# Performance work log

Hardware: AMD Instinct MI355X
Metric: run time of the kernel (lower is better)

## Reference

```python
import jax, jax.numpy as jnp
import numpy as np

BITS = 50

def _xor(a, b):
    # binary XOR on {0,1} floats: a + b - 2ab
    return a + b - 2.0 * a * b

def _maj(a, b, c):
    # majority (carry-out of a full adder) on {0,1} floats
    return a * b + a * c + b * c - 2.0 * a * b * c

def setup_inputs() -> dict:
    key = jax.random.key(0)
    kA, kB = jax.random.split(key)
    N = 1_000_000
    A = jax.random.randint(kA, (N, BITS), 0, 2).astype(jnp.float32)
    B = jax.random.randint(kB, (N, BITS), 0, 2).astype(jnp.float32)
    return {"A": A, "B": B}

def reference(A, B):
    """A - B via two's complement ripple-carry: A + NOT(B) + 1, LSB first.
    Returns (result [..., 50], borrow [..., 1])."""
    not_b = 1.0 - B                      # VecNOT
    # scan over the 50 bits (sequential carry dependency)
    a_bits = jnp.moveaxis(A, -1, 0)      # [50, N]
    b_bits = jnp.moveaxis(not_b, -1, 0)  # [50, N]
    c0 = jnp.ones(A.shape[:-1], dtype=A.dtype)  # initial carry = 1

    def step(c, ab):
        a, b = ab
        s = _xor(_xor(a, b), c)          # FullAdder sum
        c_next = _maj(a, b, c)           # FullAdder carry
        return c_next, s

    c_final, sums = jax.lax.scan(step, c0, (a_bits, b_bits))
    result = jnp.moveaxis(sums, 0, -1)   # [N, 50]
    borrow = (1.0 - c_final)[..., None]  # borrow_not(carry), [N, 1]
    return result, borrow
```

## Files before the change

kernel.cpp:

```cpp
#include <hip/hip_runtime.h>


constexpr int BITS = 50;
constexpr unsigned long long MASK50 = (1ULL << BITS) - 1ULL;

__device__ __forceinline__ void gl_lds16(const float* g, float* l) {
    __builtin_amdgcn_global_load_lds(
        (const __attribute__((address_space(1))) void*)g,
        (__attribute__((address_space(3))) void*)l, 16, 0, 0);
}
__device__ __forceinline__ void gl_lds4(const float* g, float* l) {
    __builtin_amdgcn_global_load_lds(
        (const __attribute__((address_space(1))) void*)g,
        (__attribute__((address_space(3))) void*)l, 4, 0, 0);
}

__global__ __launch_bounds__(64) void Subtractor50Bit_kernel(
    const float* __restrict__ A, const float* __restrict__ B,
    float* __restrict__ out, int N)
{
    __shared__ float sA[3200];
    __shared__ float sB[3200];

    const int lane = threadIdx.x;
    const long long rowBase = (long long)blockIdx.x * 64;
    if (rowBase >= N) return;

    if (rowBase + 64 <= N) {
        const long long eBase = rowBase * BITS;
        const float* ga = A + eBase;
        const float* gb = B + eBase;

        #pragma unroll
        for (int j = 0; j < 12; ++j) gl_lds16(ga + 256 * j + 4 * lane, &sA[256 * j]);
        gl_lds4(ga + 3072 + lane, &sA[3072]);
        gl_lds4(ga + 3136 + lane, &sA[3136]);
        #pragma unroll
        for (int j = 0; j < 12; ++j) gl_lds16(gb + 256 * j + 4 * lane, &sB[256 * j]);
        gl_lds4(gb + 3072 + lane, &sB[3072]);
        gl_lds4(gb + 3136 + lane, &sB[3136]);

        asm volatile("s_waitcnt vmcnt(0)" ::: "memory");
        __builtin_amdgcn_sched_barrier(0);

        const float2* rA = (const float2*)sA + 25 * lane;
        const float2* rB = (const float2*)sB + 25 * lane;
        unsigned alo = 0, ahi = 0, blo = 0, bhi = 0;
        #pragma unroll
        for (int j = 0; j < 25; ++j) {
            float2 va = rA[j];
            float2 vb = rB[j];
            unsigned a0 = (__float_as_uint(va.x) >> 23) & 1u;
            unsigned a1 = (__float_as_uint(va.y) >> 23) & 1u;
            unsigned b0 = (__float_as_uint(vb.x) >> 23) & 1u;
            unsigned b1 = (__float_as_uint(vb.y) >> 23) & 1u;
            if (j < 16) {
                alo |= a0 << (2 * j); alo |= a1 << (2 * j + 1);
                blo |= b0 << (2 * j); blo |= b1 << (2 * j + 1);
            } else {
                ahi |= a0 << (2 * j - 32); ahi |= a1 << (2 * j - 31);
                bhi |= b0 << (2 * j - 32); bhi |= b1 << (2 * j - 31);
            }
        }
        unsigned long long av = ((unsigned long long)ahi << 32) | alo;
        unsigned long long bv = ((unsigned long long)bhi << 32) | blo;

        unsigned long long diff = (av - bv) & MASK50;
        float borrow = (av < bv) ? 1.0f : 0.0f;

        float2* wO = (float2*)sA + 25 * lane;
        #pragma unroll
        for (int j = 0; j < 25; ++j) {
            float2 o;
            o.x = (float)(unsigned)((diff >> (2 * j)) & 1ULL);
            o.y = (float)(unsigned)((diff >> (2 * j + 1)) & 1ULL);
            wO[j] = o;
        }

        const float4* sO4 = (const float4*)sA;
        float4* go4 = (float4*)(out + eBase);
        #pragma unroll
        for (int j = 0; j < 12; ++j) go4[64 * j + lane] = sO4[64 * j + lane];
        const float2* sO2 = (const float2*)(sA + 3072);
        float2* go2 = (float2*)(out + eBase + 3072);
        go2[lane] = sO2[lane];

        out[(long long)N * BITS + rowBase + lane] = borrow;
    } else {
        long long r = rowBase + lane;
        if (r < N) {
            unsigned long long av = 0, bv = 0;
            for (int k = 0; k < BITS; ++k) {
                av |= (unsigned long long)(A[r * BITS + k] != 0.0f) << k;
                bv |= (unsigned long long)(B[r * BITS + k] != 0.0f) << k;
            }
            unsigned long long diff = (av - bv) & MASK50;
            for (int k = 0; k < BITS; ++k)
                out[r * BITS + k] = (float)((diff >> k) & 1ULL);
            out[(long long)N * BITS + r] = (av < bv) ? 1.0f : 0.0f;
        }
    }
}

extern "C" void kernel_launch(void* const* d_in, const int* in_sizes, int n_in,
                              void* d_out, int out_size, void* d_ws, size_t ws_size,
                              hipStream_t stream) {
    const float* A = (const float*)d_in[0];
    const float* B = (const float*)d_in[1];
    float* out = (float*)d_out;
    const int N = in_sizes[0] / BITS;

    const int blocks = (N + 63) / 64;
    Subtractor50Bit_kernel<<<blocks, 64, 0, stream>>>(A, B, out, N);
}
```

Before: 448.8 us.

## Convert to persistent grid with double-buffered LDS prefetch of next tile

The kernel now launches a capped grid of single-wave blocks that loop over 64-row tiles. While the current tile is processed, the next tile's A and B rows are prefetched into a second LDS buffer via global_load_lds, with a partial vmcnt wait. The leftover partial tile is handled by block 0 after the loop. The aim is to overlap load latency with compute and stores, but doubling LDS per block and capping the grid lowers resident waves per CU, so fewer memory requests may be in flight.

```diff
diff --git a/kernel.cpp b/kernel.cpp
--- a/kernel.cpp
+++ b/kernel.cpp
@@ -3,6 +3,7 @@
 
 constexpr int BITS = 50;
 constexpr unsigned long long MASK50 = (1ULL << BITS) - 1ULL;
+constexpr int TILE_F = 3200;
 
 __device__ __forceinline__ void gl_lds16(const float* g, float* l) {
     __builtin_amdgcn_global_load_lds(
@@ -15,36 +16,53 @@
         (__attribute__((address_space(3))) void*)l, 4, 0, 0);
 }
 
+__device__ __forceinline__ void stage_tile(const float* ga, const float* gb,
+                                           float* la, float* lb, int lane) {
+    #pragma unroll
+    for (int j = 0; j < 12; ++j) gl_lds16(ga + 256 * j + 4 * lane, la + 256 * j);
+    gl_lds4(ga + 3072 + lane, la + 3072);
+    gl_lds4(ga + 3136 + lane, la + 3136);
+    #pragma unroll
+    for (int j = 0; j < 12; ++j) gl_lds16(gb + 256 * j + 4 * lane, lb + 256 * j);
+    gl_lds4(gb + 3072 + lane, lb + 3072);
+    gl_lds4(gb + 3136 + lane, lb + 3136);
+}
+
 __global__ __launch_bounds__(64) void Subtractor50Bit_kernel(
     const float* __restrict__ A, const float* __restrict__ B,
     float* __restrict__ out, int N)
 {
-    __shared__ float sA[3200];
-    __shared__ float sB[3200];
+    __shared__ float sA[2][TILE_F];
+    __shared__ float sB[2][TILE_F];
 
     const int lane = threadIdx.x;
-    const long long rowBase = (long long)blockIdx.x * 64;
-    if (rowBase >= N) return;
+    const long long nFull = (long long)N >> 6;
+    const long long step  = gridDim.x;
 
-    if (rowBase + 64 <= N) {
-        const long long eBase = rowBase * BITS;
-        const float* ga = A + eBase;
-        const float* gb = B + eBase;
+    long long t = blockIdx.x;
+    int par = 0;
 
-        #pragma unroll
-        for (int j = 0; j < 12; ++j) gl_lds16(ga + 256 * j + 4 * lane, &sA[256 * j]);
-        gl_lds4(ga + 3072 + lane, &sA[3072]);
-        gl_lds4(ga + 3136 + lane, &sA[3136]);
-        #pragma unroll
-        for (int j = 0; j < 12; ++j) gl_lds16(gb + 256 * j + 4 * lane, &sB[256 * j]);
-        gl_lds4(gb + 3072 + lane, &sB[3072]);
-        gl_lds4(gb + 3136 + lane, &sB[3136]);
+    if (t < nFull) {
+        stage_tile(A + t * TILE_F, B + t * TILE_F, sA[0], sB[0], lane);
+    }
 
-        asm volatile("s_waitcnt vmcnt(0)" ::: "memory");
+    for (; t < nFull; t += step, par ^= 1) {
+        const long long tn = t + step;
+
+        if (tn < nFull) {
+            __builtin_amdgcn_sched_barrier(0);
+            stage_tile(A + tn * TILE_F, B + tn * TILE_F,
+                       sA[par ^ 1], sB[par ^ 1], lane);
+            __builtin_amdgcn_sched_barrier(0);
+            asm volatile("s_waitcnt vmcnt(28)" ::: "memory");
+        } else {
+            __builtin_amdgcn_sched_barrier(0);
+            asm volatile("s_waitcnt vmcnt(0)" ::: "memory");
+        }
         __builtin_amdgcn_sched_barrier(0);
 
-        const float2* rA = (const float2*)sA + 25 * lane;
-        const float2* rB = (const float2*)sB + 25 * lane;
+        const float2* rA = (const float2*)sA[par] + 25 * lane;
+        const float2* rB = (const float2*)sB[par] + 25 * lane;
         unsigned alo = 0, ahi = 0, blo = 0, bhi = 0;
         #pragma unroll
         for (int j = 0; j < 25; ++j) {
@@ -68,7 +86,7 @@
         unsigned long long diff = (av - bv) & MASK50;
         float borrow = (av < bv) ? 1.0f : 0.0f;
 
-        float2* wO = (float2*)sA + 25 * lane;
+        float2* wO = (float2*)sA[par] + 25 * lane;
         #pragma unroll
         for (int j = 0; j < 25; ++j) {
             float2 o;
@@ -77,17 +95,20 @@
             wO[j] = o;
         }
 
-        const float4* sO4 = (const float4*)sA;
+        const long long eBase = t * TILE_F;
+        const float4* sO4 = (const float4*)sA[par];
         float4* go4 = (float4*)(out + eBase);
         #pragma unroll
         for (int j = 0; j < 12; ++j) go4[64 * j + lane] = sO4[64 * j + lane];
-        const float2* sO2 = (const float2*)(sA + 3072);
+        const float2* sO2 = (const float2*)(sA[par] + 3072);
         float2* go2 = (float2*)(out + eBase + 3072);
         go2[lane] = sO2[lane];
 
-        out[(long long)N * BITS + rowBase + lane] = borrow;
-    } else {
-        long long r = rowBase + lane;
+        out[(long long)N * BITS + t * 64 + lane] = borrow;
+    }
+
+    if (blockIdx.x == 0) {
+        long long r = nFull * 64 + lane;
         if (r < N) {
             unsigned long long av = 0, bv = 0;
             for (int k = 0; k < BITS; ++k) {
@@ -110,6 +131,7 @@
     float* out = (float*)d_out;
     const int N = in_sizes[0] / BITS;
 
-    const int blocks = (N + 63) / 64;
-    Subtractor50Bit_kernel<<<blocks, 64, 0, stream>>>(A, B, out, N);
+    const long long nFull = (long long)N >> 6;
+    long long want = nFull < 768 ? (nFull > 0 ? nFull : 1) : 768;
+    Subtractor50Bit_kernel<<<(int)want, 64, 0, stream>>>(A, B, out, N);
 }
```

New measurement: 450.1 us. Within noise of the previous version (+0.3%).
